# Kernel tuning notes

Measured on AMD Instinct MI355X. Metric: run time of the kernel, lower is better.

The kernel has to match this reference:

```python
import jax, jax.numpy as jnp
import numpy as np

CHEB_K = 3
HIDDEN = 64
HORIZON = 12
H_FSIZE = 64                      # conv kernel width along the hidden axis
H_FILTER = HORIZON * H_FSIZE      # 768, forced by h.view(N,1,horizon,1,h_filter_size)
N_NODE = 1024
BATCH = 64
T_IN = 12
K2 = (CHEB_K * HIDDEN) ** 2       # 36864, hyp Linear in_features


def setup_inputs() -> dict:
    key = jax.random.key(0)
    k1, k2, k3, k4 = jax.random.split(key, 4)
    output = jax.random.normal(k1, (BATCH, T_IN, N_NODE, HIDDEN), jnp.float32)
    weights = jax.random.normal(k2, (N_NODE, K2), jnp.float32)
    # hyp Linear parameters (torch default init scale ~ 1/sqrt(fan_in))
    W_hyp = jax.random.normal(k3, (H_FILTER, K2), jnp.float32) / np.sqrt(K2).astype(np.float32)
    b_hyp = jax.random.normal(k4, (H_FILTER,), jnp.float32) / np.sqrt(K2).astype(np.float32)
    return {"output": output, "weights": weights, "W_hyp": W_hyp, "b_hyp": b_hyp}


def reference(output, weights, W_hyp, b_hyp):
    B, T, N, D = output.shape
    x = output[:, -1]                              # (B, N, D)   last time step
    w = weights.reshape(N, -1)                     # (N, K2)
    h = w @ W_hyp.T + b_hyp                        # (N, h_filter) hypernet Linear
    h = h.reshape(N, HORIZON, H_FSIZE)             # per-node, per-horizon 1xF filters
    Wout = D - H_FSIZE + 1                         # valid conv width (=1 here)
    # sliding windows of x along D: (B, N, Wout, F)
    idx = jnp.arange(Wout)[:, None] + jnp.arange(H_FSIZE)[None, :]
    xw = x[:, :, idx]
    # grouped conv2d (groups=N, 1 in-ch / horizon out-ch per group) == per-node contraction.
    # The torch sum(dim=3) is over a size-1 axis (no-op). Final layout (B, horizon, N, Wout).
    out = jnp.einsum('bnwf,ntf->btnw', xw, h)
    return out
```

## Files before the change

kernel.cpp:

```cpp
#include <hip/hip_runtime.h>
#include <hip/hip_bf16.h>
#include <cstdint>
#include <cstddef>

#define K2V 36864
#define MN  1024
#define HF  768

typedef __attribute__((ext_vector_type(8))) short short8;
typedef __attribute__((ext_vector_type(4))) float f32x4;

__device__ __forceinline__ unsigned pk_bf2(float a, float b) {
    __hip_bfloat16 ha = __float2bfloat16(a);
    __hip_bfloat16 hb = __float2bfloat16(b);
    unsigned short ua = *reinterpret_cast<unsigned short*>(&ha);
    unsigned short ub = *reinterpret_cast<unsigned short*>(&hb);
    return (unsigned)ua | ((unsigned)ub << 16);
}

__global__ __launch_bounds__(256, 2)
void gemm_h_split(const float* __restrict__ A, const float* __restrict__ B,
                  float* __restrict__ part, int KC)
{
    __shared__ unsigned short sA[2][128 * 64];
    __shared__ unsigned short sB[2][128 * 64];

    const int tid  = threadIdx.x;
    const int lane = tid & 63;
    const int wave = tid >> 6;
    const int wm   = wave >> 1;
    const int wn   = wave & 1;

    const int mtile = blockIdx.x / 6;
    const int ntile = blockIdx.x % 6;
    const int k0    = blockIdx.y * KC;

    const float* Ap = A + (size_t)(mtile * 128) * K2V + k0;
    const float* Bp = B + (size_t)(ntile * 128) * K2V + k0;

    const int c4 = tid & 15;
    const int rt = tid >> 4;

    f32x4 acc[4][4];
    #pragma unroll
    for (int i = 0; i < 4; ++i)
        #pragma unroll
        for (int j = 0; j < 4; ++j)
            acc[i][j] = (f32x4){0.f, 0.f, 0.f, 0.f};

    float4 ra[8], rb[8];

    auto load_step = [&](int s) {
        const float* a = Ap + s * 64 + c4 * 4;
        const float* b = Bp + s * 64 + c4 * 4;
        #pragma unroll
        for (int i = 0; i < 8; ++i) {
            const int r = rt + 16 * i;
            ra[i] = *reinterpret_cast<const float4*>(a + (size_t)r * K2V);
            rb[i] = *reinterpret_cast<const float4*>(b + (size_t)r * K2V);
        }
    };
    auto write_step = [&](int buf) {
        #pragma unroll
        for (int i = 0; i < 8; ++i) {
            const int r = rt + 16 * i;
            int off = r * 128 + c4 * 8;
            off ^= (r & 7) << 4;
            uint2 va = { pk_bf2(ra[i].x, ra[i].y), pk_bf2(ra[i].z, ra[i].w) };
            uint2 vb = { pk_bf2(rb[i].x, rb[i].y), pk_bf2(rb[i].z, rb[i].w) };
            *reinterpret_cast<uint2*>(reinterpret_cast<char*>(sA[buf]) + off) = va;
            *reinterpret_cast<uint2*>(reinterpret_cast<char*>(sB[buf]) + off) = vb;
        }
    };

    const int nsteps = KC >> 6;

    load_step(0);
    write_step(0);
    __syncthreads();

    for (int s = 0; s < nsteps; ++s) {
        if (s + 1 < nsteps) load_step(s + 1);
        const int buf = s & 1;
        #pragma unroll
        for (int ks = 0; ks < 2; ++ks) {
            short8 av[4], bv[4];
            const int cb = (ks * 32 + (lane >> 4) * 8) * 2;
            #pragma unroll
            for (int i = 0; i < 4; ++i) {
                const int rA = wm * 64 + i * 16 + (lane & 15);
                const int rB = wn * 64 + i * 16 + (lane & 15);
                int oa = rA * 128 + cb; oa ^= (rA & 7) << 4;
                int ob = rB * 128 + cb; ob ^= (rB & 7) << 4;
                av[i] = *reinterpret_cast<const short8*>(reinterpret_cast<const char*>(sA[buf]) + oa);
                bv[i] = *reinterpret_cast<const short8*>(reinterpret_cast<const char*>(sB[buf]) + ob);
            }
            #pragma unroll
            for (int i = 0; i < 4; ++i)
                #pragma unroll
                for (int j = 0; j < 4; ++j)
                    acc[i][j] = __builtin_amdgcn_mfma_f32_16x16x32_bf16(av[i], bv[j], acc[i][j], 0, 0, 0);
        }
        if (s + 1 < nsteps) write_step((s + 1) & 1);
        __syncthreads();
    }

    float* P = part + ((size_t)blockIdx.y * MN + mtile * 128 + wm * 64) * HF
                    + ntile * 128 + wn * 64;
    #pragma unroll
    for (int i = 0; i < 4; ++i) {
        #pragma unroll
        for (int j = 0; j < 4; ++j) {
            const int col = j * 16 + (lane & 15);
            #pragma unroll
            for (int q = 0; q < 4; ++q) {
                const int row = i * 16 + (lane >> 4) * 4 + q;
                P[(size_t)row * HF + col] = acc[i][j][q];
            }
        }
    }
}

__global__ __launch_bounds__(256)
void hyper_out(const float* __restrict__ xall, const float* __restrict__ part,
               const float* __restrict__ bias, float* __restrict__ out, int ksplit)
{
    const int n   = blockIdx.x;
    const int tid = threadIdx.x;
    __shared__ float hs[HF];
    __shared__ float xs[64 * 65];

    #pragma unroll
    for (int jj = 0; jj < 3; ++jj) {
        const int j = tid + jj * 256;
        float s = bias[j];
        for (int k = 0; k < ksplit; ++k)
            s += part[((size_t)k * MN + n) * HF + j];
        hs[j] = s;
    }
    {
        const int c4 = tid & 15;
        const int bt = tid >> 4;
        #pragma unroll
        for (int i = 0; i < 4; ++i) {
            const int b = bt + 16 * i;
            const float4 v = *reinterpret_cast<const float4*>(
                xall + ((size_t)(b * 12 + 11) * MN + n) * 64 + c4 * 4);
            xs[b * 65 + c4 * 4 + 0] = v.x;
            xs[b * 65 + c4 * 4 + 1] = v.y;
            xs[b * 65 + c4 * 4 + 2] = v.z;
            xs[b * 65 + c4 * 4 + 3] = v.w;
        }
    }
    __syncthreads();

    const int b  = tid & 63;
    const int t0 = tid >> 6;
    float a0 = 0.f, a1 = 0.f, a2 = 0.f;
    #pragma unroll
    for (int f = 0; f < 64; ++f) {
        const float x = xs[b * 65 + f];
        a0 += x * hs[t0 * 64 + f];
        a1 += x * hs[(t0 + 4) * 64 + f];
        a2 += x * hs[(t0 + 8) * 64 + f];
    }
    out[((size_t)(b * 12 + t0)) * MN + n]     = a0;
    out[((size_t)(b * 12 + t0 + 4)) * MN + n] = a1;
    out[((size_t)(b * 12 + t0 + 8)) * MN + n] = a2;
}

extern "C" void kernel_launch(void* const* d_in, const int* in_sizes, int n_in,
                              void* d_out, int out_size, void* d_ws, size_t ws_size,
                              hipStream_t stream)
{
    const float* xall = (const float*)d_in[0];
    const float* wts  = (const float*)d_in[1];
    const float* Whyp = (const float*)d_in[2];
    const float* bhyp = (const float*)d_in[3];
    float* out  = (float*)d_out;
    float* part = (float*)d_ws;

    const size_t slice = (size_t)MN * HF * sizeof(float);
    int ks = 1;
    const int opts[8] = {16, 12, 8, 6, 4, 3, 2, 1};
    for (int i = 0; i < 8; ++i) {
        if ((size_t)opts[i] * slice <= ws_size) { ks = opts[i]; break; }
    }
    const int KC = K2V / ks;

    dim3 g1(48, ks);
    gemm_h_split<<<g1, dim3(256), 0, stream>>>(wts, Whyp, part, KC);
    hyper_out<<<dim3(1024), dim3(256), 0, stream>>>(xall, part, bhyp, out, ks);
}
```

Baseline: 534.8 us.

## Use 8-wave GEMM blocks, XCD-aware tile mapping, and separate split-K reduction

The GEMM block grows to 512 threads (8 waves in a 2x4 layout, each wave computing 64x32), which halves per-thread accumulators and staging registers so more waves can be resident. Blocks are linearized into a 1D grid and remapped so that each XCD handles one M-tile, which improves L2 reuse of the A rows across the N and K tiles. The split-K partial sum, previously serialized per thread inside hyper_out, moves to a separate vectorized h_reduce kernel that writes the reduced result back into slice 0. This adds an extra kernel launch and an extra pass over memory.

```diff
diff --git a/kernel.cpp b/kernel.cpp
--- a/kernel.cpp
+++ b/kernel.cpp
@@ -18,7 +18,7 @@
     return (unsigned)ua | ((unsigned)ub << 16);
 }
 
-__global__ __launch_bounds__(256, 2)
+__global__ __launch_bounds__(512, 4)
 void gemm_h_split(const float* __restrict__ A, const float* __restrict__ B,
                   float* __restrict__ part, int KC)
 {
@@ -28,42 +28,53 @@
     const int tid  = threadIdx.x;
     const int lane = tid & 63;
     const int wave = tid >> 6;
-    const int wm   = wave >> 1;
-    const int wn   = wave & 1;
-
-    const int mtile = blockIdx.x / 6;
-    const int ntile = blockIdx.x % 6;
-    const int k0    = blockIdx.y * KC;
+    const int wm   = wave >> 2;
+    const int wn   = wave & 3;
+
+    int mtile, ntile, kidx;
+    if ((gridDim.x & 7) == 0) {
+        const int xcd = blockIdx.x & 7;
+        const int pos = blockIdx.x >> 3;
+        mtile = xcd;
+        kidx  = pos / 6;
+        ntile = pos - kidx * 6;
+    } else {
+        kidx = blockIdx.x / 48;
+        const int rem = blockIdx.x - kidx * 48;
+        mtile = rem / 6;
+        ntile = rem - mtile * 6;
+    }
+    const int k0 = kidx * KC;
 
     const float* Ap = A + (size_t)(mtile * 128) * K2V + k0;
     const float* Bp = B + (size_t)(ntile * 128) * K2V + k0;
 
     const int c4 = tid & 15;
-    const int rt = tid >> 4;
-
-    f32x4 acc[4][4];
+    const int r0 = tid >> 4;
+
+    f32x4 acc[4][2];
     #pragma unroll
     for (int i = 0; i < 4; ++i)
         #pragma unroll
-        for (int j = 0; j < 4; ++j)
+        for (int j = 0; j < 2; ++j)
             acc[i][j] = (f32x4){0.f, 0.f, 0.f, 0.f};
 
-    float4 ra[8], rb[8];
+    float4 ra[4], rb[4];
 
     auto load_step = [&](int s) {
         const float* a = Ap + s * 64 + c4 * 4;
         const float* b = Bp + s * 64 + c4 * 4;
         #pragma unroll
-        for (int i = 0; i < 8; ++i) {
-            const int r = rt + 16 * i;
+        for (int i = 0; i < 4; ++i) {
+            const int r = r0 + 32 * i;
             ra[i] = *reinterpret_cast<const float4*>(a + (size_t)r * K2V);
             rb[i] = *reinterpret_cast<const float4*>(b + (size_t)r * K2V);
         }
     };
     auto write_step = [&](int buf) {
         #pragma unroll
-        for (int i = 0; i < 8; ++i) {
-            const int r = rt + 16 * i;
+        for (int i = 0; i < 4; ++i) {
+            const int r = r0 + 32 * i;
             int off = r * 128 + c4 * 8;
             off ^= (r & 7) << 4;
             uint2 va = { pk_bf2(ra[i].x, ra[i].y), pk_bf2(ra[i].z, ra[i].w) };
@@ -84,33 +95,36 @@
         const int buf = s & 1;
         #pragma unroll
         for (int ks = 0; ks < 2; ++ks) {
-            short8 av[4], bv[4];
+            short8 av[4], bv[2];
             const int cb = (ks * 32 + (lane >> 4) * 8) * 2;
             #pragma unroll
             for (int i = 0; i < 4; ++i) {
                 const int rA = wm * 64 + i * 16 + (lane & 15);
-                const int rB = wn * 64 + i * 16 + (lane & 15);
                 int oa = rA * 128 + cb; oa ^= (rA & 7) << 4;
+                av[i] = *reinterpret_cast<const short8*>(reinterpret_cast<const char*>(sA[buf]) + oa);
+            }
+            #pragma unroll
+            for (int j = 0; j < 2; ++j) {
+                const int rB = wn * 32 + j * 16 + (lane & 15);
                 int ob = rB * 128 + cb; ob ^= (rB & 7) << 4;
-                av[i] = *reinterpret_cast<const short8*>(reinterpret_cast<const char*>(sA[buf]) + oa);
-                bv[i] = *reinterpret_cast<const short8*>(reinterpret_cast<const char*>(sB[buf]) + ob);
+                bv[j] = *reinterpret_cast<const short8*>(reinterpret_cast<const char*>(sB[buf]) + ob);
             }
             #pragma unroll
             for (int i = 0; i < 4; ++i)
                 #pragma unroll
-                for (int j = 0; j < 4; ++j)
+                for (int j = 0; j < 2; ++j)
                     acc[i][j] = __builtin_amdgcn_mfma_f32_16x16x32_bf16(av[i], bv[j], acc[i][j], 0, 0, 0);
         }
         if (s + 1 < nsteps) write_step((s + 1) & 1);
         __syncthreads();
     }
 
-    float* P = part + ((size_t)blockIdx.y * MN + mtile * 128 + wm * 64) * HF
-                    + ntile * 128 + wn * 64;
+    float* P = part + ((size_t)kidx * MN + mtile * 128 + wm * 64) * HF
+                    + ntile * 128 + wn * 32;
     #pragma unroll
     for (int i = 0; i < 4; ++i) {
         #pragma unroll
-        for (int j = 0; j < 4; ++j) {
+        for (int j = 0; j < 2; ++j) {
             const int col = j * 16 + (lane & 15);
             #pragma unroll
             for (int q = 0; q < 4; ++q) {
@@ -122,8 +136,42 @@
 }
 
 __global__ __launch_bounds__(256)
-void hyper_out(const float* __restrict__ xall, const float* __restrict__ part,
-               const float* __restrict__ bias, float* __restrict__ out, int ksplit)
+void h_reduce(float* __restrict__ part, const float* __restrict__ bias, int ksplit)
+{
+    const int fidx = blockIdx.x * 256 + threadIdx.x;
+    const int n  = fidx / 192;
+    const int j4 = fidx - n * 192;
+    const size_t base = (size_t)n * HF + j4 * 4;
+    const size_t kstride = (size_t)MN * HF;
+
+    float4 s0 = *reinterpret_cast<const float4*>(bias + j4 * 4);
+    float4 s1 = {0.f, 0.f, 0.f, 0.f}, s2 = {0.f, 0.f, 0.f, 0.f}, s3 = {0.f, 0.f, 0.f, 0.f};
+    int k = 0;
+    for (; k + 4 <= ksplit; k += 4) {
+        float4 p0 = *reinterpret_cast<const float4*>(part + (size_t)(k + 0) * kstride + base);
+        float4 p1 = *reinterpret_cast<const float4*>(part + (size_t)(k + 1) * kstride + base);
+        float4 p2 = *reinterpret_cast<const float4*>(part + (size_t)(k + 2) * kstride + base);
+        float4 p3 = *reinterpret_cast<const float4*>(part + (size_t)(k + 3) * kstride + base);
+        s0.x += p0.x; s0.y += p0.y; s0.z += p0.z; s0.w += p0.w;
+        s1.x += p1.x; s1.y += p1.y; s1.z += p1.z; s1.w += p1.w;
+        s2.x += p2.x; s2.y += p2.y; s2.z += p2.z; s2.w += p2.w;
+        s3.x += p3.x; s3.y += p3.y; s3.z += p3.z; s3.w += p3.w;
+    }
+    for (; k < ksplit; ++k) {
+        float4 p0 = *reinterpret_cast<const float4*>(part + (size_t)k * kstride + base);
+        s0.x += p0.x; s0.y += p0.y; s0.z += p0.z; s0.w += p0.w;
+    }
+    float4 r;
+    r.x = (s0.x + s1.x) + (s2.x + s3.x);
+    r.y = (s0.y + s1.y) + (s2.y + s3.y);
+    r.z = (s0.z + s1.z) + (s2.z + s3.z);
+    r.w = (s0.w + s1.w) + (s2.w + s3.w);
+    *reinterpret_cast<float4*>(part + base) = r;
+}
+
+__global__ __launch_bounds__(256)
+void hyper_out(const float* __restrict__ xall, const float* __restrict__ hred,
+               float* __restrict__ out)
 {
     const int n   = blockIdx.x;
     const int tid = threadIdx.x;
@@ -133,10 +181,7 @@
     #pragma unroll
     for (int jj = 0; jj < 3; ++jj) {
         const int j = tid + jj * 256;
-        float s = bias[j];
-        for (int k = 0; k < ksplit; ++k)
-            s += part[((size_t)k * MN + n) * HF + j];
-        hs[j] = s;
+        hs[j] = hred[(size_t)n * HF + j];
     }
     {
         const int c4 = tid & 15;
@@ -188,7 +233,7 @@
     }
     const int KC = K2V / ks;
 
-    dim3 g1(48, ks);
-    gemm_h_split<<<g1, dim3(256), 0, stream>>>(wts, Whyp, part, KC);
-    hyper_out<<<dim3(1024), dim3(256), 0, stream>>>(xall, part, bhyp, out, ks);
-}
+    gemm_h_split<<<dim3(48 * ks), dim3(512), 0, stream>>>(wts, Whyp, part, KC);
+    h_reduce<<<dim3(768), dim3(256), 0, stream>>>(part, bhyp, ks);
+    hyper_out<<<dim3(1024), dim3(256), 0, stream>>>(xall, part, out);
+}
```

New measurement: 509.1 us. 1.05x faster.
